# Kernel tuning notes

Hardware: AMD Instinct MI355X
Metric: run time of the kernel (lower is better)

## Reference

```python
import jax, jax.numpy as jnp
import numpy as np

N_NODES = 100000
N_EDGES = 1600000
NIN = 128
NH = 128
NOUT = 1
N_MID_LAYERS = 9  # layers 1-9 (128->128); layer 10 is 128->1


def _spmm(adj_vals, edge_src, edge_dst, x):
    # out[dst] += adj_vals * x[src]   (sparse adj @ x, COO)
    msgs = adj_vals[:, None] * x[edge_src]          # [E, d]
    return jax.ops.segment_sum(msgs, edge_dst, num_segments=N_NODES)


def setup_inputs() -> dict:
    key = jax.random.key(0)
    ks = jax.random.split(key, 8)
    features = jax.random.normal(ks[0], (N_NODES, NIN), dtype=jnp.float32)
    adj_vals = jax.random.uniform(ks[1], (N_EDGES,), dtype=jnp.float32)
    Ws = jax.random.normal(ks[2], (N_MID_LAYERS, NH, NH), dtype=jnp.float32) * 0.05
    bs = jax.random.normal(ks[3], (N_MID_LAYERS, NH), dtype=jnp.float32) * 0.05
    W10 = jax.random.normal(ks[4], (NH, NOUT), dtype=jnp.float32) * 0.05
    b10 = jax.random.normal(ks[5], (NOUT,), dtype=jnp.float32) * 0.05
    edge_src = jax.random.randint(ks[6], (N_EDGES,), 0, N_NODES, dtype=jnp.int32)
    edge_dst = jax.random.randint(ks[7], (N_EDGES,), 0, N_NODES, dtype=jnp.int32)
    return {"features": features, "adj_vals": adj_vals, "Ws": Ws, "bs": bs,
            "W10": W10, "b10": b10, "edge_src": edge_src, "edge_dst": edge_dst}


def reference(features, adj_vals, Ws, bs, W10, b10, edge_src, edge_dst):
    x = features
    # layers 1-9: relu(spmm(adj, x @ W) + b)
    for i in range(N_MID_LAYERS):
        support = x @ Ws[i]                               # [N, NH] dense GEMM
        x = jax.nn.relu(_spmm(adj_vals, edge_src, edge_dst, support) + bs[i])
    # layer 10 (no relu), then log_softmax over flattened output
    support = x @ W10                                     # [N, NOUT]
    out = _spmm(adj_vals, edge_src, edge_dst, support) + b10
    return jax.nn.log_softmax(out.reshape(-1))            # [N*NOUT]
```

## Files before the change

kernel.cpp:

```cpp
#include <hip/hip_runtime.h>
#include <float.h>

#define NN 100000
#define NE 1600000
#define NH 128
#define N_MID 9
#define NBKT ((NN + 255) / 256)
#define P1_EPB 4096
#define NP1B ((NE + P1_EPB - 1) / P1_EPB)
#define P2_CAP 5120

typedef _Float16 half8 __attribute__((ext_vector_type(8)));
typedef float f32x4 __attribute__((ext_vector_type(4)));


__global__ __launch_bounds__(256) void conv_w(const float* __restrict__ W, _Float16* __restrict__ Wt) {
    int i = blockIdx.x * 256 + threadIdx.x;
    if (i >= N_MID * NH * NH) return;
    int l = i / (NH * NH), rem = i % (NH * NH);
    int n = rem / NH, k = rem % NH;
    Wt[i] = (_Float16)W[l * NH * NH + k * NH + n];
}


__global__ __launch_bounds__(256) void bhist_k(const int* __restrict__ edst, int* __restrict__ bh) {
    __shared__ int hist[NBKT];
    const int tid = threadIdx.x;
    for (int i = tid; i < NBKT; i += 256) hist[i] = 0;
    __syncthreads();
    const int e0 = blockIdx.x * P1_EPB;
    const int e1 = min(e0 + P1_EPB, NE);
    for (int e = e0 + tid; e < e1; e += 256) atomicAdd(&hist[edst[e] >> 8], 1);
    __syncthreads();
    for (int i = tid; i < NBKT; i += 256) bh[blockIdx.x * NBKT + i] = hist[i];
}

__global__ __launch_bounds__(512) void bscan_cols(const int* __restrict__ bh, int* __restrict__ obh,
                                                  int* __restrict__ btot) {
    __shared__ int s[512];
    const int b = blockIdx.x, tid = threadIdx.x;
    int v = (tid < NP1B) ? bh[tid * NBKT + b] : 0;
    s[tid] = v;
    __syncthreads();
    for (int off = 1; off < 512; off <<= 1) {
        int t = (tid >= off) ? s[tid - off] : 0;
        __syncthreads();
        s[tid] += t;
        __syncthreads();
    }
    if (tid < NP1B) obh[tid * NBKT + b] = s[tid] - v;
    if (tid == NP1B - 1) btot[b] = s[tid];
}

__global__ __launch_bounds__(512) void bscan_top(const int* __restrict__ btot, int* __restrict__ bbase) {
    __shared__ int s[512];
    const int tid = threadIdx.x;
    int v = (tid < NBKT) ? btot[tid] : 0;
    s[tid] = v;
    __syncthreads();
    for (int off = 1; off < 512; off <<= 1) {
        int t = (tid >= off) ? s[tid - off] : 0;
        __syncthreads();
        s[tid] += t;
        __syncthreads();
    }
    if (tid < NBKT) bbase[tid] = s[tid] - v;
    if (tid == NBKT - 1) bbase[NBKT] = s[tid];
}

__global__ __launch_bounds__(256) void p1_bucket(const int* __restrict__ esrc, const int* __restrict__ edst,
                                                 const float* __restrict__ av, const int* __restrict__ bbase,
                                                 const int* __restrict__ obh, int2* __restrict__ gbuf) {
    __shared__ int base[NBKT];
    __shared__ int rnk[NBKT];
    const int tid = threadIdx.x;
    for (int i = tid; i < NBKT; i += 256) {
        base[i] = bbase[i] + obh[blockIdx.x * NBKT + i];
        rnk[i] = 0;
    }
    __syncthreads();
    const int e0 = blockIdx.x * P1_EPB;
    const int e1 = min(e0 + P1_EPB, NE);
    for (int e = e0 + tid; e < e1; e += 256) {
        int d = edst[e];
        int b = d >> 8;
        int r = atomicAdd(&rnk[b], 1);
        gbuf[base[b] + r] = make_int2(esrc[e] | ((d & 255) << 24), __float_as_int(av[e]));
    }
}

__global__ __launch_bounds__(256) void p2_sort(const int2* __restrict__ gbuf, const int* __restrict__ bbase,
                                               int* __restrict__ rp, int2* __restrict__ rec) {
    __shared__ int hist[256];
    __shared__ int sc[256];
    __shared__ int offs[256];
    __shared__ int r2[256];
    __shared__ int2 buf[P2_CAP];
    const int b = blockIdx.x;
    const int tid = threadIdx.x;
    const int n0 = b * 256;
    const int e0 = bbase[b];
    const int e1 = bbase[b + 1];
    const int n = e1 - e0;
    hist[tid] = 0; r2[tid] = 0;
    __syncthreads();
    for (int i = tid; i < n; i += 256) atomicAdd(&hist[(unsigned)gbuf[e0 + i].x >> 24], 1);
    __syncthreads();
    sc[tid] = hist[tid];
    __syncthreads();
    for (int off = 1; off < 256; off <<= 1) {
        int t = (tid >= off) ? sc[tid - off] : 0;
        __syncthreads();
        sc[tid] += t;
        __syncthreads();
    }
    offs[tid] = sc[tid] - hist[tid];
    __syncthreads();
    if (n0 + tid < NN) rp[n0 + tid] = e0 + offs[tid];
    if (b == NBKT - 1 && tid == 0) rp[NN] = e1;
    if (n <= P2_CAP) {
        for (int i = tid; i < n; i += 256) {
            int2 rv = gbuf[e0 + i];
            int dl = (unsigned)rv.x >> 24;
            int p = offs[dl] + atomicAdd(&r2[dl], 1);
            buf[p] = make_int2(rv.x & 0x00FFFFFF, rv.y);
        }
        __syncthreads();
        for (int i = tid; i < n; i += 256) rec[e0 + i] = buf[i];
    } else {
        for (int i = tid; i < n; i += 256) {
            int2 rv = gbuf[e0 + i];
            int dl = (unsigned)rv.x >> 24;
            int p = offs[dl] + atomicAdd(&r2[dl], 1);
            rec[e0 + p] = make_int2(rv.x & 0x00FFFFFF, rv.y);
        }
    }
}


#define WLD 136

__device__ __forceinline__ void gemm_core(half8 a0, half8 a1, half8 a2, half8 a3,
                                          const _Float16* wsh, int r, int kb,
                                          int row0, _Float16* __restrict__ S) {
    f32x4 acc[8];
#pragma unroll
    for (int t = 0; t < 8; t++) acc[t] = (f32x4){0.f, 0.f, 0.f, 0.f};
#pragma unroll
    for (int t = 0; t < 8; t++) {
        const _Float16* wp = wsh + (16 * t + r) * WLD + kb * 8;
        half8 b0 = *(const half8*)(wp);
        half8 b1 = *(const half8*)(wp + 32);
        half8 b2 = *(const half8*)(wp + 64);
        half8 b3 = *(const half8*)(wp + 96);
        acc[t] = __builtin_amdgcn_mfma_f32_16x16x32_f16(a0, b0, acc[t], 0, 0, 0);
        acc[t] = __builtin_amdgcn_mfma_f32_16x16x32_f16(a1, b1, acc[t], 0, 0, 0);
        acc[t] = __builtin_amdgcn_mfma_f32_16x16x32_f16(a2, b2, acc[t], 0, 0, 0);
        acc[t] = __builtin_amdgcn_mfma_f32_16x16x32_f16(a3, b3, acc[t], 0, 0, 0);
    }
    const int orow = row0 + kb * 4;
#pragma unroll
    for (int j = 0; j < 4; j++) {
        if (orow + j < NN) {
            _Float16* sp = S + (size_t)(orow + j) * NH + r;
#pragma unroll
            for (int t = 0; t < 8; t++) sp[16 * t] = (_Float16)acc[t][j];
        }
    }
}

__global__ __launch_bounds__(256) void gemm_mfma(const _Float16* __restrict__ X, const _Float16* __restrict__ Wt,
                                                 _Float16* __restrict__ S) {
    __shared__ _Float16 wsh[128 * WLD];
    const int tid = threadIdx.x;
    for (int c = tid; c < 2048; c += 256) {
        int row = c >> 4, col = c & 15;
        *(half8*)&wsh[row * WLD + col * 8] = *(const half8*)&Wt[row * 128 + col * 8];
    }
    const int wid = tid >> 6;
    const int lane = tid & 63;
    const int r = lane & 15, kb = lane >> 4;
    const int row0 = blockIdx.x * 64 + wid * 16;
    int arow = row0 + r;
    if (arow >= NN) arow = NN - 1;
    const _Float16* xp = X + (size_t)arow * NH + kb * 8;
    half8 a0 = *(const half8*)(xp);
    half8 a1 = *(const half8*)(xp + 32);
    half8 a2 = *(const half8*)(xp + 64);
    half8 a3 = *(const half8*)(xp + 96);
    __syncthreads();
    gemm_core(a0, a1, a2, a3, wsh, r, kb, row0, S);
}

__global__ __launch_bounds__(256) void gemm_mfma_f32(const float* __restrict__ X, const _Float16* __restrict__ Wt,
                                                     _Float16* __restrict__ S) {
    __shared__ _Float16 wsh[128 * WLD];
    const int tid = threadIdx.x;
    for (int c = tid; c < 2048; c += 256) {
        int row = c >> 4, col = c & 15;
        *(half8*)&wsh[row * WLD + col * 8] = *(const half8*)&Wt[row * 128 + col * 8];
    }
    const int wid = tid >> 6;
    const int lane = tid & 63;
    const int r = lane & 15, kb = lane >> 4;
    const int row0 = blockIdx.x * 64 + wid * 16;
    int arow = row0 + r;
    if (arow >= NN) arow = NN - 1;
    const float* xp = X + (size_t)arow * NH + kb * 8;
    half8 a[4];
#pragma unroll
    for (int s = 0; s < 4; s++) {
        float4 f0 = *(const float4*)(xp + 32 * s);
        float4 f1 = *(const float4*)(xp + 32 * s + 4);
        a[s][0] = (_Float16)f0.x; a[s][1] = (_Float16)f0.y;
        a[s][2] = (_Float16)f0.z; a[s][3] = (_Float16)f0.w;
        a[s][4] = (_Float16)f1.x; a[s][5] = (_Float16)f1.y;
        a[s][6] = (_Float16)f1.z; a[s][7] = (_Float16)f1.w;
    }
    __syncthreads();
    gemm_core(a[0], a[1], a[2], a[3], wsh, r, kb, row0, S);
}


__global__ __launch_bounds__(256) void spmm_f16(const _Float16* __restrict__ S, const int2* __restrict__ rec,
                                                const int* __restrict__ rp, const float* __restrict__ bias,
                                                _Float16* __restrict__ Xo, const float* __restrict__ w10,
                                                float* __restrict__ s10, int fuseDot) {
    const int wv = blockIdx.x * 4 + (threadIdx.x >> 6);
    const int node0 = wv * 4;
    if (node0 >= NN) return;
    const int lane = threadIdx.x & 63;
    const int g = lane >> 4;
    const int c = lane & 15;
    const int nEnd = min(node0 + 4, NN);
    const float4 b0 = *(const float4*)&bias[c * 8];
    const float4 b1 = *(const float4*)&bias[c * 8 + 4];

    int beg = rp[node0];
    for (int node = node0; node < nEnd; node++) {
        int end = rp[node + 1];
        float acc[8] = {0.f, 0.f, 0.f, 0.f, 0.f, 0.f, 0.f, 0.f};
        float acc2[8] = {0.f, 0.f, 0.f, 0.f, 0.f, 0.f, 0.f, 0.f};
        int e = beg + g;
        int2 n1 = make_int2(0, 0), n2 = make_int2(0, 0);
        if (e + 4 < end) { n1 = rec[e]; n2 = rec[e + 4]; }
        for (; e + 4 < end; e += 8) {
            int2 rv1 = n1, rv2 = n2;
            if (e + 12 < end) { n1 = rec[e + 8]; n2 = rec[e + 12]; }
            half8 r1 = *(const half8*)&S[(size_t)rv1.x * NH + c * 8];
            half8 r2 = *(const half8*)&S[(size_t)rv2.x * NH + c * 8];
            float v1 = __int_as_float(rv1.y);
            float v2 = __int_as_float(rv2.y);
#pragma unroll
            for (int j = 0; j < 8; j++) {
                acc[j]  = fmaf(v1, (float)r1[j], acc[j]);
                acc2[j] = fmaf(v2, (float)r2[j], acc2[j]);
            }
        }
        if (e < end) {
            int2 rv = rec[e];
            float v = __int_as_float(rv.y);
            half8 r1 = *(const half8*)&S[(size_t)rv.x * NH + c * 8];
#pragma unroll
            for (int j = 0; j < 8; j++) acc[j] = fmaf(v, (float)r1[j], acc[j]);
        }
#pragma unroll
        for (int j = 0; j < 8; j++) {
            acc[j] += acc2[j];
            acc[j] += __shfl_xor(acc[j], 16, 64);
            acc[j] += __shfl_xor(acc[j], 32, 64);
        }
        if (g == 0) {
            half8 o;
            o[0] = (_Float16)fmaxf(acc[0] + b0.x, 0.f);
            o[1] = (_Float16)fmaxf(acc[1] + b0.y, 0.f);
            o[2] = (_Float16)fmaxf(acc[2] + b0.z, 0.f);
            o[3] = (_Float16)fmaxf(acc[3] + b0.w, 0.f);
            o[4] = (_Float16)fmaxf(acc[4] + b1.x, 0.f);
            o[5] = (_Float16)fmaxf(acc[5] + b1.y, 0.f);
            o[6] = (_Float16)fmaxf(acc[6] + b1.z, 0.f);
            o[7] = (_Float16)fmaxf(acc[7] + b1.w, 0.f);
            if (!fuseDot) {
                *(half8*)&Xo[(size_t)node * NH + c * 8] = o;
            } else {
                float4 wa = *(const float4*)&w10[c * 8];
                float4 wb = *(const float4*)&w10[c * 8 + 4];
                float p = (float)o[0] * wa.x + (float)o[1] * wa.y + (float)o[2] * wa.z + (float)o[3] * wa.w
                        + (float)o[4] * wb.x + (float)o[5] * wb.y + (float)o[6] * wb.z + (float)o[7] * wb.w;
#pragma unroll
                for (int off = 8; off; off >>= 1) p += __shfl_xor(p, off, 64);
                if (c == 0) s10[node] = p;
            }
        }
        beg = end;
    }
}


__global__ __launch_bounds__(256) void spmm_scalar(const float* __restrict__ s10, const int2* __restrict__ rec,
                                                   const int* __restrict__ rp, const float* __restrict__ b10,
                                                   float* __restrict__ o10) {
    int node = blockIdx.x * 256 + threadIdx.x;
    if (node >= NN) return;
    int beg = rp[node], end = rp[node + 1];
    float a = 0.f;
    for (int e = beg; e < end; e++) {
        int2 r = rec[e];
        a = fmaf(__int_as_float(r.y), s10[r.x], a);
    }
    o10[node] = a + b10[0];
}

#define LSM_NB 240

__global__ __launch_bounds__(256) void lsm_max(const float* __restrict__ v, float* __restrict__ pmax) {
    __shared__ float s[256];
    float m = -FLT_MAX;
    for (int i = blockIdx.x * 256 + threadIdx.x; i < NN; i += LSM_NB * 256) m = fmaxf(m, v[i]);
    s[threadIdx.x] = m;
    __syncthreads();
    for (int off = 128; off; off >>= 1) {
        if (threadIdx.x < off) s[threadIdx.x] = fmaxf(s[threadIdx.x], s[threadIdx.x + off]);
        __syncthreads();
    }
    if (threadIdx.x == 0) pmax[blockIdx.x] = s[0];
}

__global__ __launch_bounds__(256) void lsm_sum(const float* __restrict__ v, const float* __restrict__ pmax,
                                               float* __restrict__ psum) {
    __shared__ float s[256];
    float m = -FLT_MAX;
    if (threadIdx.x < LSM_NB) m = pmax[threadIdx.x];
    s[threadIdx.x] = m;
    __syncthreads();
    for (int off = 128; off; off >>= 1) {
        if (threadIdx.x < off) s[threadIdx.x] = fmaxf(s[threadIdx.x], s[threadIdx.x + off]);
        __syncthreads();
    }
    float gm = s[0];
    __syncthreads();
    float sum = 0.f;
    for (int i = blockIdx.x * 256 + threadIdx.x; i < NN; i += LSM_NB * 256) sum += expf(v[i] - gm);
    s[threadIdx.x] = sum;
    __syncthreads();
    for (int off = 128; off; off >>= 1) {
        if (threadIdx.x < off) s[threadIdx.x] += s[threadIdx.x + off];
        __syncthreads();
    }
    if (threadIdx.x == 0) psum[blockIdx.x] = s[0];
}

__global__ __launch_bounds__(256) void lsm_fin(const float* __restrict__ pmax, const float* __restrict__ psum,
                                               float* __restrict__ c) {
    __shared__ float s[256];
    float m = -FLT_MAX, sum = 0.f;
    if (threadIdx.x < LSM_NB) { m = pmax[threadIdx.x]; sum = psum[threadIdx.x]; }
    s[threadIdx.x] = m;
    __syncthreads();
    for (int off = 128; off; off >>= 1) {
        if (threadIdx.x < off) s[threadIdx.x] = fmaxf(s[threadIdx.x], s[threadIdx.x + off]);
        __syncthreads();
    }
    float gm = s[0];
    __syncthreads();
    s[threadIdx.x] = sum;
    __syncthreads();
    for (int off = 128; off; off >>= 1) {
        if (threadIdx.x < off) s[threadIdx.x] += s[threadIdx.x + off];
        __syncthreads();
    }
    if (threadIdx.x == 0) c[0] = gm + logf(s[0]);
}

__global__ __launch_bounds__(256) void lsm_write(const float* __restrict__ o10, const float* __restrict__ c,
                                                 float* __restrict__ out) {
    int i = blockIdx.x * 256 + threadIdx.x;
    if (i < NN) out[i] = o10[i] - c[0];
}


extern "C" void kernel_launch(void* const* d_in, const int* in_sizes, int n_in,
                              void* d_out, int out_size, void* d_ws, size_t ws_size,
                              hipStream_t stream) {
    const float* features = (const float*)d_in[0];
    const float* adj_vals = (const float*)d_in[1];
    const float* Ws       = (const float*)d_in[2];
    const float* bs       = (const float*)d_in[3];
    const float* W10      = (const float*)d_in[4];
    const float* b10      = (const float*)d_in[5];
    const int*   esrc     = (const int*)d_in[6];
    const int*   edst     = (const int*)d_in[7];
    float* out = (float*)d_out;

    char* ws = (char*)d_ws;
    const size_t SZH = (size_t)NN * NH * 2;
    _Float16* S_h = (_Float16*)(ws);
    _Float16* xA  = (_Float16*)(ws + SZH);
    _Float16* xB  = (_Float16*)(ws + 2 * SZH);
    _Float16* Wt  = (_Float16*)(ws + 3 * SZH);
    char* p = ws + 3 * SZH + (size_t)N_MID * NH * NH * 2;
    int2* rec  = (int2*)p;
    int2* gbuf = (int2*)(p + (size_t)NE * 8);
    int* bh    = (int*)(p + 2 * (size_t)NE * 8);
    int* obh   = bh + NP1B * NBKT;
    int* btot  = obh + NP1B * NBKT;
    int* bbase = btot + NBKT;
    int* rp    = bbase + NBKT + 1;
    float* s10 = (float*)(rp + NN + 1);
    float* o10 = s10 + NN;
    float* pmax = o10 + NN;
    float* psum = pmax + LSM_NB;
    float* cbuf = psum + LSM_NB;

    conv_w<<<(N_MID * NH * NH + 255) / 256, 256, 0, stream>>>(Ws, Wt);

    bhist_k<<<NP1B, 256, 0, stream>>>(edst, bh);
    bscan_cols<<<NBKT, 512, 0, stream>>>(bh, obh, btot);
    bscan_top<<<1, 512, 0, stream>>>(btot, bbase);
    p1_bucket<<<NP1B, 256, 0, stream>>>(esrc, edst, adj_vals, bbase, obh, gbuf);
    p2_sort<<<NBKT, 256, 0, stream>>>(gbuf, bbase, rp, rec);

    gemm_mfma_f32<<<(NN + 63) / 64, 256, 0, stream>>>(features, Wt, S_h);
    spmm_f16<<<(NN + 15) / 16, 256, 0, stream>>>(S_h, rec, rp, bs, xA, nullptr, nullptr, 0);

    const _Float16* xin = xA;
    _Float16* xout = xB;
    for (int l = 1; l < N_MID; l++) {
        gemm_mfma<<<(NN + 63) / 64, 256, 0, stream>>>(xin, Wt + (size_t)l * NH * NH, S_h);
        int fuse = (l == N_MID - 1) ? 1 : 0;
        spmm_f16<<<(NN + 15) / 16, 256, 0, stream>>>(S_h, rec, rp, bs + (size_t)l * NH, xout, W10, s10, fuse);
        xin = xout;
        xout = (xout == xA) ? xB : xA;
    }

    spmm_scalar<<<(NN + 255) / 256, 256, 0, stream>>>(s10, rec, rp, b10, o10);
    lsm_max<<<LSM_NB, 256, 0, stream>>>(o10, pmax);
    lsm_sum<<<LSM_NB, 256, 0, stream>>>(o10, pmax, psum);
    lsm_fin<<<1, 256, 0, stream>>>(pmax, psum, cbuf);
    lsm_write<<<(NN + 255) / 256, 256, 0, stream>>>(o10, cbuf, out);
}
```

Measured before the change: 745.9 us.

## Store GEMM output in column-block layout and gather per 16-column slice in SpMM

The GEMM can now write its fp16 output as eight column blocks of 16 columns each (one [N,16] slab per block). A new SpMM kernel assigns one block per column slice, so that for each slice the gathered S rows occupy a 3.2 MB slab, which is intended to fit in cache and make the random gathers mostly cache hits. Each node is handled by 16 lanes with two edge streams and prefetching of edge records. The last mid layer keeps the old row-major path because it fuses the W10 dot product. The trade-off is that edge records are read eight times, once per column block, and the output stores are narrower.

```diff
diff --git a/kernel.cpp b/kernel.cpp
--- a/kernel.cpp
+++ b/kernel.cpp
@@ -140,6 +140,7 @@
 
 #define WLD 136
 
+template <int COLBLK>
 __device__ __forceinline__ void gemm_core(half8 a0, half8 a1, half8 a2, half8 a3,
                                           const _Float16* wsh, int r, int kb,
                                           int row0, _Float16* __restrict__ S) {
@@ -161,14 +162,18 @@
     const int orow = row0 + kb * 4;
 #pragma unroll
     for (int j = 0; j < 4; j++) {
-        if (orow + j < NN) {
-            _Float16* sp = S + (size_t)(orow + j) * NH + r;
-#pragma unroll
-            for (int t = 0; t < 8; t++) sp[16 * t] = (_Float16)acc[t][j];
-        }
-    }
-}
-
+        int row = orow + j;
+        if (row < NN) {
+#pragma unroll
+            for (int t = 0; t < 8; t++) {
+                if (COLBLK) S[((size_t)t * NN + row) * 16 + r] = (_Float16)acc[t][j];
+                else        S[(size_t)row * NH + 16 * t + r]   = (_Float16)acc[t][j];
+            }
+        }
+    }
+}
+
+template <int COLBLK>
 __global__ __launch_bounds__(256) void gemm_mfma(const _Float16* __restrict__ X, const _Float16* __restrict__ Wt,
                                                  _Float16* __restrict__ S) {
     __shared__ _Float16 wsh[128 * WLD];
@@ -189,9 +194,10 @@
     half8 a2 = *(const half8*)(xp + 64);
     half8 a3 = *(const half8*)(xp + 96);
     __syncthreads();
-    gemm_core(a0, a1, a2, a3, wsh, r, kb, row0, S);
-}
-
+    gemm_core<COLBLK>(a0, a1, a2, a3, wsh, r, kb, row0, S);
+}
+
+template <int COLBLK>
 __global__ __launch_bounds__(256) void gemm_mfma_f32(const float* __restrict__ X, const _Float16* __restrict__ Wt,
                                                      _Float16* __restrict__ S) {
     __shared__ _Float16 wsh[128 * WLD];
@@ -218,7 +224,80 @@
         a[s][6] = (_Float16)f1.z; a[s][7] = (_Float16)f1.w;
     }
     __syncthreads();
-    gemm_core(a[0], a[1], a[2], a[3], wsh, r, kb, row0, S);
+    gemm_core<COLBLK>(a[0], a[1], a[2], a[3], wsh, r, kb, row0, S);
+}
+
+
+__global__ __launch_bounds__(256) void spmm_cs(const _Float16* __restrict__ S, const int2* __restrict__ rec,
+                                               const int* __restrict__ rp, const float* __restrict__ bias,
+                                               _Float16* __restrict__ Xo) {
+    const int cb = blockIdx.x & 7;
+    const int chunk = blockIdx.x >> 3;
+    const int wid = threadIdx.x >> 6;
+    const int lane = threadIdx.x & 63;
+    const int h  = lane & 1;
+    const int eg = (lane >> 1) & 7;
+    const int ns = lane >> 4;
+    const int node = chunk * 16 + wid * 4 + ns;
+    if (node >= NN) return;
+    const _Float16* Sb = S + (size_t)cb * NN * 16;
+
+    const int beg = rp[node], end = rp[node + 1];
+    float acc[8] = {0.f, 0.f, 0.f, 0.f, 0.f, 0.f, 0.f, 0.f};
+    float acc2[8] = {0.f, 0.f, 0.f, 0.f, 0.f, 0.f, 0.f, 0.f};
+    int e = beg + eg;
+    long long n1 = 0, n2 = 0;
+    if (e + 8 < end) {
+        n1 = __builtin_nontemporal_load((const long long*)(rec + e));
+        n2 = __builtin_nontemporal_load((const long long*)(rec + e + 8));
+    }
+    for (; e + 8 < end; e += 16) {
+        long long r1 = n1, r2 = n2;
+        if (e + 24 < end) {
+            n1 = __builtin_nontemporal_load((const long long*)(rec + e + 16));
+            n2 = __builtin_nontemporal_load((const long long*)(rec + e + 24));
+        }
+        int s1 = (int)(r1 & 0xffffffffLL);
+        int s2 = (int)(r2 & 0xffffffffLL);
+        float v1 = __int_as_float((int)(r1 >> 32));
+        float v2 = __int_as_float((int)(r2 >> 32));
+        half8 x1 = *(const half8*)&Sb[(size_t)s1 * 16 + h * 8];
+        half8 x2 = *(const half8*)&Sb[(size_t)s2 * 16 + h * 8];
+#pragma unroll
+        for (int j = 0; j < 8; j++) {
+            acc[j]  = fmaf(v1, (float)x1[j], acc[j]);
+            acc2[j] = fmaf(v2, (float)x2[j], acc2[j]);
+        }
+    }
+    if (e < end) {
+        int2 rv = rec[e];
+        float v = __int_as_float(rv.y);
+        half8 x1 = *(const half8*)&Sb[(size_t)rv.x * 16 + h * 8];
+#pragma unroll
+        for (int j = 0; j < 8; j++) acc[j] = fmaf(v, (float)x1[j], acc[j]);
+    }
+#pragma unroll
+    for (int j = 0; j < 8; j++) {
+        acc[j] += acc2[j];
+        acc[j] += __shfl_xor(acc[j], 2, 64);
+        acc[j] += __shfl_xor(acc[j], 4, 64);
+        acc[j] += __shfl_xor(acc[j], 8, 64);
+    }
+    if (eg == 0) {
+        const int col0 = cb * 16 + h * 8;
+        float4 ba = *(const float4*)&bias[col0];
+        float4 bb = *(const float4*)&bias[col0 + 4];
+        half8 o;
+        o[0] = (_Float16)fmaxf(acc[0] + ba.x, 0.f);
+        o[1] = (_Float16)fmaxf(acc[1] + ba.y, 0.f);
+        o[2] = (_Float16)fmaxf(acc[2] + ba.z, 0.f);
+        o[3] = (_Float16)fmaxf(acc[3] + ba.w, 0.f);
+        o[4] = (_Float16)fmaxf(acc[4] + bb.x, 0.f);
+        o[5] = (_Float16)fmaxf(acc[5] + bb.y, 0.f);
+        o[6] = (_Float16)fmaxf(acc[6] + bb.z, 0.f);
+        o[7] = (_Float16)fmaxf(acc[7] + bb.w, 0.f);
+        *(half8*)&Xo[(size_t)node * NH + col0] = o;
+    }
 }
 
 
@@ -420,18 +499,23 @@
     p1_bucket<<<NP1B, 256, 0, stream>>>(esrc, edst, adj_vals, bbase, obh, gbuf);
     p2_sort<<<NBKT, 256, 0, stream>>>(gbuf, bbase, rp, rec);
 
-    gemm_mfma_f32<<<(NN + 63) / 64, 256, 0, stream>>>(features, Wt, S_h);
-    spmm_f16<<<(NN + 15) / 16, 256, 0, stream>>>(S_h, rec, rp, bs, xA, nullptr, nullptr, 0);
+    const int CS_GRID = ((NN + 15) / 16) * 8;
+
+    gemm_mfma_f32<1><<<(NN + 63) / 64, 256, 0, stream>>>(features, Wt, S_h);
+    spmm_cs<<<CS_GRID, 256, 0, stream>>>(S_h, rec, rp, bs, xA);
 
     const _Float16* xin = xA;
     _Float16* xout = xB;
-    for (int l = 1; l < N_MID; l++) {
-        gemm_mfma<<<(NN + 63) / 64, 256, 0, stream>>>(xin, Wt + (size_t)l * NH * NH, S_h);
-        int fuse = (l == N_MID - 1) ? 1 : 0;
-        spmm_f16<<<(NN + 15) / 16, 256, 0, stream>>>(S_h, rec, rp, bs + (size_t)l * NH, xout, W10, s10, fuse);
+    for (int l = 1; l < N_MID - 1; l++) {
+        gemm_mfma<1><<<(NN + 63) / 64, 256, 0, stream>>>(xin, Wt + (size_t)l * NH * NH, S_h);
+        spmm_cs<<<CS_GRID, 256, 0, stream>>>(S_h, rec, rp, bs + (size_t)l * NH, xout);
         xin = xout;
         xout = (xout == xA) ? xB : xA;
     }
+
+    gemm_mfma<0><<<(NN + 63) / 64, 256, 0, stream>>>(xin, Wt + (size_t)(N_MID - 1) * NH * NH, S_h);
+    spmm_f16<<<(NN + 15) / 16, 256, 0, stream>>>(S_h, rec, rp, bs + (size_t)(N_MID - 1) * NH,
+                                                 xout, W10, s10, 1);
 
     spmm_scalar<<<(NN + 255) / 256, 256, 0, stream>>>(s10, rec, rp, b10, o10);
     lsm_max<<<LSM_NB, 256, 0, stream>>>(o10, pmax);
```

Result: slower. 1.456 ms (+95.2%).
